# Kernel tuning notes

Hardware: AMD Instinct MI355X
Metric: run time of the kernel (lower is better)

Reference implementation:

```python
import jax, jax.numpy as jnp
import numpy as np

NUM_HEADS = 16
HEAD_DIM = 64  # att_output_dim // num_heads = 1024 // 16


def setup_inputs() -> dict:
    key = jax.random.key(0)
    ks = jax.random.split(key, 7)
    B, S, D_IN, D_OUT = 4, 2048, 1024, 1024
    std = 1.0 / np.sqrt(D_IN)
    return {
        "ts10_input": jax.random.normal(ks[0], (B, S, D_IN), dtype=jnp.float32),
        "Wq": jax.random.uniform(ks[1], (D_IN, D_OUT), jnp.float32, -std, std),
        "bq": jax.random.uniform(ks[2], (D_OUT,), jnp.float32, -std, std),
        "Wk": jax.random.uniform(ks[3], (D_IN, D_OUT), jnp.float32, -std, std),
        "bk": jax.random.uniform(ks[4], (D_OUT,), jnp.float32, -std, std),
        "Wv": jax.random.uniform(ks[5], (D_IN, D_OUT), jnp.float32, -std, std),
        "bv": jax.random.uniform(ks[6], (D_OUT,), jnp.float32, -std, std),
        "mask": 1,
    }


def reference(ts10_input, Wq, bq, Wk, bk, Wv, bv, mask):
    B, S, _ = ts10_input.shape
    H, Dh = NUM_HEADS, HEAD_DIM

    def split_heads(x):  # (B,S,H*Dh) -> (B,H,S,Dh)
        return x.reshape(B, S, H, Dh).transpose(0, 2, 1, 3)

    q = split_heads(ts10_input @ Wq + bq)
    k = split_heads(ts10_input @ Wk + bk)
    v = split_heads(ts10_input @ Wv + bv)

    scores = jnp.einsum("bhqd,bhkd->bhqk", q, k) / jnp.sqrt(jnp.float32(Dh))
    if mask:
        causal = jnp.tril(jnp.ones((S, S), dtype=bool))  # keep lower triangle incl diag
        scores = jnp.where(causal, scores, -jnp.inf)
    probs = jax.nn.softmax(scores, axis=-1)
    ctx = jnp.einsum("bhqk,bhkd->bhqd", probs, v)
    return ctx.transpose(0, 2, 1, 3).reshape(B, S, H * Dh)
```

## Files before the change

### kernel.cpp

```cpp
#include <hip/hip_runtime.h>

typedef __bf16 bf16x8 __attribute__((ext_vector_type(8)));
typedef __bf16 bf16x4 __attribute__((ext_vector_type(4)));
typedef short s16x4 __attribute__((ext_vector_type(4)));
typedef float f32x4 __attribute__((ext_vector_type(4)));
typedef unsigned short u16x8 __attribute__((ext_vector_type(8)));
typedef unsigned short u16x4 __attribute__((ext_vector_type(4)));
typedef unsigned int u32x2 __attribute__((ext_vector_type(2)));
typedef unsigned int u32x4 __attribute__((ext_vector_type(4)));
typedef unsigned int __attribute__((address_space(1))) as1_uint;
typedef unsigned int __attribute__((address_space(3))) as3_uint;

#define S_LEN 2048
#define NB 4
#define NH 16
#define HD 64
#define DM 1024

#define Q_SCALE 0.18033688011112042f

__device__ __forceinline__ unsigned short f2bf(float f) {
  union { float f; unsigned int u; } v; v.f = f;
  unsigned int r = v.u + 0x7fffu + ((v.u >> 16) & 1u);
  return (unsigned short)(r >> 16);
}

__device__ __forceinline__ unsigned int fbits(float f) {
  union { float f; unsigned int u; } v; v.f = f;
  return v.u;
}

__device__ __forceinline__ f32x4 mfma16(u16x4 a, u16x4 b, f32x4 c) {
#if __has_builtin(__builtin_amdgcn_mfma_f32_16x16x16_bf16)
  return __builtin_amdgcn_mfma_f32_16x16x16_bf16(
      __builtin_bit_cast(bf16x4, a), __builtin_bit_cast(bf16x4, b), c, 0, 0, 0);
#else
  return __builtin_amdgcn_mfma_f32_16x16x16bf16_1k(
      __builtin_bit_cast(s16x4, a), __builtin_bit_cast(s16x4, b), c, 0, 0, 0);
#endif
}

__global__ __launch_bounds__(256) void cvt_x(const float* __restrict__ x,
                                             unsigned short* __restrict__ xb) {
  int i = (blockIdx.x * 256 + threadIdx.x) * 8;
  f32x4 a = *(const f32x4*)(x + i);
  f32x4 b = *(const f32x4*)(x + i + 4);
  u16x8 o;
  o[0] = f2bf(a[0]); o[1] = f2bf(a[1]); o[2] = f2bf(a[2]); o[3] = f2bf(a[3]);
  o[4] = f2bf(b[0]); o[5] = f2bf(b[1]); o[6] = f2bf(b[2]); o[7] = f2bf(b[3]);
  *(u16x8*)(xb + i) = o;
}

__global__ __launch_bounds__(256) void cvt_wt(const float* __restrict__ Wq,
                                              const float* __restrict__ Wk,
                                              const float* __restrict__ Wv,
                                              unsigned short* __restrict__ wt) {
  const float* W = (blockIdx.z == 0) ? Wq : (blockIdx.z == 1) ? Wk : Wv;
  unsigned short* WT = wt + (size_t)blockIdx.z * DM * DM;
  __shared__ float tile[32][33];
  int tx = threadIdx.x & 31, ty = threadIdx.x >> 5;
  int k0 = blockIdx.x * 32, n0 = blockIdx.y * 32;
#pragma unroll
  for (int i = 0; i < 4; ++i)
    tile[ty + 8 * i][tx] = W[(size_t)(k0 + ty + 8 * i) * DM + n0 + tx];
  __syncthreads();
#pragma unroll
  for (int i = 0; i < 4; ++i)
    WT[(size_t)(n0 + ty + 8 * i) * DM + k0 + tx] = f2bf(tile[tx][ty + 8 * i]);
}

__global__ __launch_bounds__(256, 4) void qkv_gemm(const unsigned short* __restrict__ xb,
                                                   const unsigned short* __restrict__ wt,
                                                   const float* __restrict__ bq,
                                                   const float* __restrict__ bk,
                                                   const float* __restrict__ bv,
                                                   unsigned short* __restrict__ qo,
                                                   unsigned short* __restrict__ ko,
                                                   unsigned short* __restrict__ vto) {
  const int z = blockIdx.z;
  const unsigned short* WT = wt + (size_t)z * DM * DM;
  const float* bias = (z == 0) ? bq : (z == 1) ? bk : bv;
  const int m0 = blockIdx.x * 128;
  const int n0 = blockIdx.y * 128;
  __shared__ __align__(16) unsigned short Lds[128 * 136];
  unsigned short* Al = Lds;
  unsigned short* Bl = Lds + 128 * 64;
  const int tid = threadIdx.x;
  const int wave = tid >> 6, lane = tid & 63, quad = lane >> 4, lw = lane & 15;
  const int wm = (wave >> 1) * 64, wn = (wave & 1) * 64;

  f32x4 acc[4][4];
#pragma unroll
  for (int mt = 0; mt < 4; ++mt)
#pragma unroll
    for (int nt = 0; nt < 4; ++nt) acc[mt][nt] = (f32x4){0.f, 0.f, 0.f, 0.f};

  for (int k0 = 0; k0 < DM; k0 += 64) {
    __syncthreads();
#pragma unroll
    for (int i = 0; i < 4; ++i) {
      int idx = i * 256 + tid;
      int r = idx >> 3, cp = idx & 7;
      int cl = cp ^ (r & 7);
      const unsigned short* ga = xb + (size_t)(m0 + r) * DM + k0 + cl * 8;
      __builtin_amdgcn_global_load_lds((const as1_uint*)ga, (as3_uint*)(Al + idx * 8), 16, 0, 0);
      const unsigned short* gb = WT + (size_t)(n0 + r) * DM + k0 + cl * 8;
      __builtin_amdgcn_global_load_lds((const as1_uint*)gb, (as3_uint*)(Bl + idx * 8), 16, 0, 0);
    }
    __syncthreads();
#pragma unroll
    for (int kc = 0; kc < 2; ++kc) {
      bf16x8 af[4], bfr[4];
#pragma unroll
      for (int mt = 0; mt < 4; ++mt) {
        int r = wm + mt * 16 + lw;
        int cp = (kc * 4 + quad) ^ (r & 7);
        af[mt] = *(const bf16x8*)(Al + r * 64 + cp * 8);
      }
#pragma unroll
      for (int nt = 0; nt < 4; ++nt) {
        int r = wn + nt * 16 + lw;
        int cp = (kc * 4 + quad) ^ (r & 7);
        bfr[nt] = *(const bf16x8*)(Bl + r * 64 + cp * 8);
      }
#pragma unroll
      for (int mt = 0; mt < 4; ++mt)
#pragma unroll
        for (int nt = 0; nt < 4; ++nt)
          acc[mt][nt] = __builtin_amdgcn_mfma_f32_16x16x32_bf16(af[mt], bfr[nt], acc[mt][nt], 0, 0, 0);
    }
  }

  float bias4[4];
#pragma unroll
  for (int nt = 0; nt < 4; ++nt) bias4[nt] = bias[n0 + wn + nt * 16 + lw];

  __syncthreads();

  if (z < 2) {
    const float sc = (z == 0) ? Q_SCALE : 1.0f;
#pragma unroll
    for (int mt = 0; mt < 4; ++mt)
#pragma unroll
      for (int nt = 0; nt < 4; ++nt) {
        int n = wn + nt * 16 + lw;
#pragma unroll
        for (int r = 0; r < 4; ++r) {
          int m = wm + mt * 16 + quad * 4 + r;
          Lds[m * 136 + n] = f2bf((acc[mt][nt][r] + bias4[nt]) * sc);
        }
      }
    __syncthreads();
    unsigned short* dst = (z == 0) ? qo : ko;
    const int rr = tid >> 1;
    const int cbase = (tid & 1) * 64;
    const int m = m0 + rr;
    const int b = m >> 11, s = m & 2047;
#pragma unroll
    for (int ch = 0; ch < 8; ++ch) {
      int cc = cbase + ch * 8;
      int n = n0 + cc;
      int h = n >> 6, d = n & 63;
      u32x4 v = *(const u32x4*)(Lds + rr * 136 + cc);
      *(u32x4*)(dst + ((size_t)(b * NH + h) * S_LEN + s) * HD + d) = v;
    }
  } else {
#pragma unroll
    for (int mt = 0; mt < 4; ++mt)
#pragma unroll
      for (int nt = 0; nt < 4; ++nt) {
        int n = wn + nt * 16 + lw;
        int mb = wm + mt * 16 + quad * 4;
        u16x4 pk;
#pragma unroll
        for (int r = 0; r < 4; ++r) pk[r] = f2bf(acc[mt][nt][r] + bias4[nt]);
        *(u16x4*)(Lds + n * 136 + mb) = pk;
      }
    __syncthreads();
    const int rr = tid >> 1;
    const int cbase = (tid & 1) * 64;
    const int n = n0 + rr;
    const int h = n >> 6, d = n & 63;
#pragma unroll
    for (int ch = 0; ch < 8; ++ch) {
      int cc = cbase + ch * 8;
      int m = m0 + cc;
      int b = m >> 11, s = m & 2047;
      u32x4 v = *(const u32x4*)(Lds + rr * 136 + cc);
      *(u32x4*)(vto + ((size_t)(b * NH + h) * HD + d) * S_LEN + s) = v;
    }
  }
}

__global__ __launch_bounds__(256, 4) void attn(const unsigned short* __restrict__ Qb,
                                               const unsigned short* __restrict__ Kb,
                                               const unsigned short* __restrict__ Vtb,
                                               float* __restrict__ out) {
  const int flat = blockIdx.x;
  const int bh_lo = flat & 7;
  const int qpair = (flat >> 3) & 15;
  const int bh_hi = flat >> 7;
  const int bh = bh_lo + 8 * bh_hi;
  const int b = bh >> 4, h = bh & 15;
  const int tid = threadIdx.x;
  const int wave = tid >> 6, lane = tid & 63;
  const int quad = lane >> 4, lw = lane & 15;
  const int qlo = qpair * 64;
  const int qhi = (31 - qpair) * 64;
  const unsigned short* Qp = Qb + (size_t)bh * S_LEN * HD;
  const unsigned short* Kp = Kb + (size_t)bh * S_LEN * HD;
  const unsigned short* Vp = Vtb + (size_t)bh * HD * S_LEN;

  __shared__ __align__(16) unsigned short Kl[2][64 * 64];
  __shared__ __align__(16) unsigned short Vl[2][64 * 64];

  bf16x8 aq[2][2];
#pragma unroll
  for (int rg = 0; rg < 2; ++rg) {
    const int qbase = rg ? qhi : qlo;
#pragma unroll
    for (int kc = 0; kc < 2; ++kc)
      aq[rg][kc] = *(const bf16x8*)(Qp + (size_t)(qbase + wave * 16 + lw) * HD + kc * 32 + quad * 8);
  }

  u16x4 ones4;
#pragma unroll
  for (int i = 0; i < 4; ++i) ones4[i] = 0x3F80;

  f32x4 accO[2][4];
  f32x4 accL[2];
#pragma unroll
  for (int rg = 0; rg < 2; ++rg) {
    accL[rg] = (f32x4){0.f, 0.f, 0.f, 0.f};
#pragma unroll
    for (int dg = 0; dg < 4; ++dg) accO[rg][dg] = (f32x4){0.f, 0.f, 0.f, 0.f};
  }

  const int qr0 = qlo + wave * 16 + lw;
  const int qr1 = qhi + wave * 16 + lw;

  const int T = 32 - qpair;

  {
#pragma unroll
    for (int i = 0; i < 2; ++i) {
      int idx = i * 256 + tid;
      int r = idx >> 3, c = (idx & 7) ^ (r & 7);
      __builtin_amdgcn_global_load_lds((const as1_uint*)(Kp + (size_t)r * HD + c * 8),
                                       (as3_uint*)(Kl[0] + idx * 8), 16, 0, 0);
      __builtin_amdgcn_global_load_lds((const as1_uint*)(Vp + (size_t)r * S_LEN + c * 8),
                                       (as3_uint*)(Vl[0] + idx * 8), 16, 0, 0);
    }
  }

  for (int t = 0; t < T; ++t) {
    const int kv = t * 64;
    const int cur = t & 1;
    __syncthreads();

    if (t + 1 < T) {
      const int kvn = kv + 64;
#pragma unroll
      for (int i = 0; i < 2; ++i) {
        int idx = i * 256 + tid;
        int r = idx >> 3, c = (idx & 7) ^ (r & 7);
        __builtin_amdgcn_global_load_lds((const as1_uint*)(Kp + (size_t)(kvn + r) * HD + c * 8),
                                         (as3_uint*)(Kl[cur ^ 1] + idx * 8), 16, 0, 0);
        __builtin_amdgcn_global_load_lds((const as1_uint*)(Vp + (size_t)r * S_LEN + kvn + c * 8),
                                         (as3_uint*)(Vl[cur ^ 1] + idx * 8), 16, 0, 0);
      }
    }

    const bool a0 = (t <= qpair);
    const bool d0 = (t == qpair);
    const bool d1 = (t == T - 1);

#pragma unroll
    for (int g = 0; g < 4; ++g) {
      const unsigned short* kp = Kl[cur] + (g * 16 + lw) * 64;
      const int sw = lw & 7;
      bf16x8 kf0 = *(const bf16x8*)(kp + ((quad ^ sw) * 8));
      bf16x8 kf1 = *(const bf16x8*)(kp + (((4 + quad) ^ sw) * 8));

      u16x4 pf[2];
#pragma unroll
      for (int rg = 0; rg < 2; ++rg) {
        if (rg == 0 && !a0) continue;
        f32x4 s = (f32x4){0.f, 0.f, 0.f, 0.f};
        s = __builtin_amdgcn_mfma_f32_16x16x32_bf16(kf0, aq[rg][0], s, 0, 0, 0);
        s = __builtin_amdgcn_mfma_f32_16x16x32_bf16(kf1, aq[rg][1], s, 0, 0, 0);
        const bool dg_ = rg ? d1 : d0;
        const int qr = rg ? qr1 : qr0;
        if (dg_) {
#pragma unroll
          for (int r = 0; r < 4; ++r) {
            float e = __builtin_amdgcn_exp2f(s[r]);
            s[r] = (kv + g * 16 + quad * 4 + r > qr) ? 0.f : e;
          }
        } else {
#pragma unroll
          for (int r = 0; r < 4; ++r) s[r] = __builtin_amdgcn_exp2f(s[r]);
        }
        u32x2 pk;
        pk[0] = (fbits(s[1]) & 0xFFFF0000u) | (fbits(s[0]) >> 16);
        pk[1] = (fbits(s[3]) & 0xFFFF0000u) | (fbits(s[2]) >> 16);
        pf[rg] = __builtin_bit_cast(u16x4, pk);
      }

#pragma unroll
      for (int dg = 0; dg < 4; ++dg) {
        const int row = dg * 16 + lw;
        const int slot = (2 * g + (quad >> 1)) ^ (lw & 7);
        u16x4 vf = *(const u16x4*)(Vl[cur] + row * 64 + slot * 8 + (quad & 1) * 4);
        if (a0) accO[0][dg] = mfma16(pf[0], vf, accO[0][dg]);
        accO[1][dg] = mfma16(pf[1], vf, accO[1][dg]);
      }
      if (a0) accL[0] = mfma16(pf[0], ones4, accL[0]);
      accL[1] = mfma16(pf[1], ones4, accL[1]);
    }
  }

#pragma unroll
  for (int rg = 0; rg < 2; ++rg) {
    const int qbase = rg ? qhi : qlo;
    float* op = out + ((size_t)b * S_LEN + qbase + wave * 16 + quad * 4) * DM + h * HD + lw;
#pragma unroll
    for (int r = 0; r < 4; ++r) {
      float inv = 1.0f / accL[rg][r];
#pragma unroll
      for (int dg = 0; dg < 4; ++dg) op[(size_t)r * DM + dg * 16] = accO[rg][dg][r] * inv;
    }
  }
}

extern "C" void kernel_launch(void* const* d_in, const int* in_sizes, int n_in,
                              void* d_out, int out_size, void* d_ws, size_t ws_size,
                              hipStream_t stream) {
  const float* x = (const float*)d_in[0];
  const float* Wq = (const float*)d_in[1];
  const float* bq = (const float*)d_in[2];
  const float* Wk = (const float*)d_in[3];
  const float* bk = (const float*)d_in[4];
  const float* Wv = (const float*)d_in[5];
  const float* bv = (const float*)d_in[6];
  float* out = (float*)d_out;

  char* ws = (char*)d_ws;
  unsigned short* xb = (unsigned short*)(ws + 0);
  unsigned short* wt = (unsigned short*)(ws + 16777216);
  unsigned short* qb = (unsigned short*)(ws + 23068672);
  unsigned short* kb = (unsigned short*)(ws + 39845888);
  unsigned short* vt = (unsigned short*)(ws + 56623104);

  hipLaunchKernelGGL(cvt_x, dim3(4096), dim3(256), 0, stream, x, xb);
  hipLaunchKernelGGL(cvt_wt, dim3(32, 32, 3), dim3(256), 0, stream, Wq, Wk, Wv, wt);
  hipLaunchKernelGGL(qkv_gemm, dim3(64, 8, 3), dim3(256), 0, stream,
                     xb, wt, bq, bk, bv, qb, kb, vt);
  hipLaunchKernelGGL(attn, dim3(1024), dim3(256), 0, stream, qb, kb, vt, out);
}
```

Measured before the change: 230.1 us.

## Double-buffer QKV GEMM LDS staging and merge conversion kernels into one launch

The QKV GEMM K-loop now uses two 32-wide LDS buffers, issuing the next tile's global-to-LDS loads before computing on the current one. This drops one barrier per iteration and overlaps memory with MFMA work. It also changes the swizzle pattern to fit the narrower tile. Separately, the x conversion and weight transpose-conversion kernels are fused into one launch, which removes one kernel launch at the cost of a branch per block. The LDS layout reuse and the smaller K step double the loop iterations, so per-iteration overhead goes up.

After: 226.0 us. About the same (-1.8%).

```diff
diff --git a/kernel.cpp b/kernel.cpp
--- a/kernel.cpp
+++ b/kernel.cpp
@@ -40,33 +40,36 @@
 #endif
 }
 
-__global__ __launch_bounds__(256) void cvt_x(const float* __restrict__ x,
-                                             unsigned short* __restrict__ xb) {
-  int i = (blockIdx.x * 256 + threadIdx.x) * 8;
-  f32x4 a = *(const f32x4*)(x + i);
-  f32x4 b = *(const f32x4*)(x + i + 4);
-  u16x8 o;
-  o[0] = f2bf(a[0]); o[1] = f2bf(a[1]); o[2] = f2bf(a[2]); o[3] = f2bf(a[3]);
-  o[4] = f2bf(b[0]); o[5] = f2bf(b[1]); o[6] = f2bf(b[2]); o[7] = f2bf(b[3]);
-  *(u16x8*)(xb + i) = o;
-}
-
-__global__ __launch_bounds__(256) void cvt_wt(const float* __restrict__ Wq,
-                                              const float* __restrict__ Wk,
-                                              const float* __restrict__ Wv,
-                                              unsigned short* __restrict__ wt) {
-  const float* W = (blockIdx.z == 0) ? Wq : (blockIdx.z == 1) ? Wk : Wv;
-  unsigned short* WT = wt + (size_t)blockIdx.z * DM * DM;
+__global__ __launch_bounds__(256) void prep(const float* __restrict__ x,
+                                            unsigned short* __restrict__ xb,
+                                            const float* __restrict__ Wq,
+                                            const float* __restrict__ Wk,
+                                            const float* __restrict__ Wv,
+                                            unsigned short* __restrict__ wt) {
   __shared__ float tile[32][33];
-  int tx = threadIdx.x & 31, ty = threadIdx.x >> 5;
-  int k0 = blockIdx.x * 32, n0 = blockIdx.y * 32;
-#pragma unroll
-  for (int i = 0; i < 4; ++i)
-    tile[ty + 8 * i][tx] = W[(size_t)(k0 + ty + 8 * i) * DM + n0 + tx];
-  __syncthreads();
-#pragma unroll
-  for (int i = 0; i < 4; ++i)
-    WT[(size_t)(n0 + ty + 8 * i) * DM + k0 + tx] = f2bf(tile[tx][ty + 8 * i]);
+  if (blockIdx.x < 4096) {
+    int i = (blockIdx.x * 256 + threadIdx.x) * 8;
+    f32x4 a = *(const f32x4*)(x + i);
+    f32x4 b = *(const f32x4*)(x + i + 4);
+    u16x8 o;
+    o[0] = f2bf(a[0]); o[1] = f2bf(a[1]); o[2] = f2bf(a[2]); o[3] = f2bf(a[3]);
+    o[4] = f2bf(b[0]); o[5] = f2bf(b[1]); o[6] = f2bf(b[2]); o[7] = f2bf(b[3]);
+    *(u16x8*)(xb + i) = o;
+  } else {
+    int id = blockIdx.x - 4096;
+    int z = id >> 10, r = id & 1023;
+    const float* W = (z == 0) ? Wq : (z == 1) ? Wk : Wv;
+    unsigned short* WT = wt + (size_t)z * DM * DM;
+    int k0 = (r & 31) * 32, n0 = (r >> 5) * 32;
+    int tx = threadIdx.x & 31, ty = threadIdx.x >> 5;
+#pragma unroll
+    for (int i = 0; i < 4; ++i)
+      tile[ty + 8 * i][tx] = W[(size_t)(k0 + ty + 8 * i) * DM + n0 + tx];
+    __syncthreads();
+#pragma unroll
+    for (int i = 0; i < 4; ++i)
+      WT[(size_t)(n0 + ty + 8 * i) * DM + k0 + tx] = f2bf(tile[tx][ty + 8 * i]);
+  }
 }
 
 __global__ __launch_bounds__(256, 4) void qkv_gemm(const unsigned short* __restrict__ xb,
@@ -83,8 +86,6 @@
   const int m0 = blockIdx.x * 128;
   const int n0 = blockIdx.y * 128;
   __shared__ __align__(16) unsigned short Lds[128 * 136];
-  unsigned short* Al = Lds;
-  unsigned short* Bl = Lds + 128 * 64;
   const int tid = threadIdx.x;
   const int wave = tid >> 6, lane = tid & 63, quad = lane >> 4, lw = lane & 15;
   const int wm = (wave >> 1) * 64, wn = (wave & 1) * 64;
@@ -95,40 +96,45 @@
 #pragma unroll
     for (int nt = 0; nt < 4; ++nt) acc[mt][nt] = (f32x4){0.f, 0.f, 0.f, 0.f};
 
-  for (int k0 = 0; k0 < DM; k0 += 64) {
-    __syncthreads();
-#pragma unroll
-    for (int i = 0; i < 4; ++i) {
-      int idx = i * 256 + tid;
-      int r = idx >> 3, cp = idx & 7;
-      int cl = cp ^ (r & 7);
-      const unsigned short* ga = xb + (size_t)(m0 + r) * DM + k0 + cl * 8;
-      __builtin_amdgcn_global_load_lds((const as1_uint*)ga, (as3_uint*)(Al + idx * 8), 16, 0, 0);
-      const unsigned short* gb = WT + (size_t)(n0 + r) * DM + k0 + cl * 8;
-      __builtin_amdgcn_global_load_lds((const as1_uint*)gb, (as3_uint*)(Bl + idx * 8), 16, 0, 0);
-    }
-    __syncthreads();
-#pragma unroll
-    for (int kc = 0; kc < 2; ++kc) {
-      bf16x8 af[4], bfr[4];
-#pragma unroll
-      for (int mt = 0; mt < 4; ++mt) {
-        int r = wm + mt * 16 + lw;
-        int cp = (kc * 4 + quad) ^ (r & 7);
-        af[mt] = *(const bf16x8*)(Al + r * 64 + cp * 8);
-      }
-#pragma unroll
-      for (int nt = 0; nt < 4; ++nt) {
-        int r = wn + nt * 16 + lw;
-        int cp = (kc * 4 + quad) ^ (r & 7);
-        bfr[nt] = *(const bf16x8*)(Bl + r * 64 + cp * 8);
-      }
-#pragma unroll
-      for (int mt = 0; mt < 4; ++mt)
-#pragma unroll
-        for (int nt = 0; nt < 4; ++nt)
-          acc[mt][nt] = __builtin_amdgcn_mfma_f32_16x16x32_bf16(af[mt], bfr[nt], acc[mt][nt], 0, 0, 0);
-    }
+  auto stage = [&](int k0, int buf) {
+    unsigned short* Al = Lds + buf * 4096;
+    unsigned short* Bl = Lds + 8192 + buf * 4096;
+#pragma unroll
+    for (int i = 0; i < 2; ++i) {
+      int c = i * 256 + tid;
+      int row = c >> 2;
+      int scn = (c & 3) ^ ((row >> 1) & 3);
+      const unsigned short* ga = xb + (size_t)(m0 + row) * DM + k0 + scn * 8;
+      __builtin_amdgcn_global_load_lds((const as1_uint*)ga, (as3_uint*)(Al + c * 8), 16, 0, 0);
+      const unsigned short* gb = WT + (size_t)(n0 + row) * DM + k0 + scn * 8;
+      __builtin_amdgcn_global_load_lds((const as1_uint*)gb, (as3_uint*)(Bl + c * 8), 16, 0, 0);
+    }
+  };
+
+  stage(0, 0);
+  for (int k0 = 0; k0 < DM; k0 += 32) {
+    const int cur = (k0 >> 5) & 1;
+    __syncthreads();
+    if (k0 + 32 < DM) stage(k0 + 32, cur ^ 1);
+
+    const unsigned short* Al = Lds + cur * 4096;
+    const unsigned short* Bl = Lds + 8192 + cur * 4096;
+    bf16x8 af[4], bfr[4];
+#pragma unroll
+    for (int mt = 0; mt < 4; ++mt) {
+      int r = wm + mt * 16 + lw;
+      af[mt] = *(const bf16x8*)(Al + r * 32 + (quad ^ ((r >> 1) & 3)) * 8);
+    }
+#pragma unroll
+    for (int nt = 0; nt < 4; ++nt) {
+      int r = wn + nt * 16 + lw;
+      bfr[nt] = *(const bf16x8*)(Bl + r * 32 + (quad ^ ((r >> 1) & 3)) * 8);
+    }
+#pragma unroll
+    for (int mt = 0; mt < 4; ++mt)
+#pragma unroll
+      for (int nt = 0; nt < 4; ++nt)
+        acc[mt][nt] = __builtin_amdgcn_mfma_f32_16x16x32_bf16(af[mt], bfr[nt], acc[mt][nt], 0, 0, 0);
   }
 
   float bias4[4];
@@ -352,8 +358,7 @@
   unsigned short* kb = (unsigned short*)(ws + 39845888);
   unsigned short* vt = (unsigned short*)(ws + 56623104);
 
-  hipLaunchKernelGGL(cvt_x, dim3(4096), dim3(256), 0, stream, x, xb);
-  hipLaunchKernelGGL(cvt_wt, dim3(32, 32, 3), dim3(256), 0, stream, Wq, Wk, Wv, wt);
+  hipLaunchKernelGGL(prep, dim3(7168), dim3(256), 0, stream, x, xb, Wq, Wk, Wv, wt);
   hipLaunchKernelGGL(qkv_gemm, dim3(64, 8, 3), dim3(256), 0, stream,
                      xb, wt, bq, bk, bv, qb, kb, vt);
   hipLaunchKernelGGL(attn, dim3(1024), dim3(256), 0, stream, qb, kb, vt, out);
```

## Merge conversion kernels and halve GEMM epilogue LDS to raise occupancy

Applied to the files above, without the earlier changes.

Combines the x-to-bf16 conversion and the weight transpose-convert into one launch, which removes a kernel launch and the gap between the two kernels. In the QKV GEMM, the epilogue staging now runs in two phases of 64 rows or columns, so LDS shrinks from 128x136 to 16384 halves and launch bounds rise to 5 blocks per SIMD group. The goal is higher GEMM occupancy. The cost is an extra pair of barriers in the epilogue, with half the waves idle during each staging phase.

New measurement: 267.7 us. 16.4% more time.

```diff
diff --git a/kernel.cpp b/kernel.cpp
--- a/kernel.cpp
+++ b/kernel.cpp
@@ -40,36 +40,39 @@
 #endif
 }
 
-__global__ __launch_bounds__(256) void cvt_x(const float* __restrict__ x,
-                                             unsigned short* __restrict__ xb) {
-  int i = (blockIdx.x * 256 + threadIdx.x) * 8;
-  f32x4 a = *(const f32x4*)(x + i);
-  f32x4 b = *(const f32x4*)(x + i + 4);
-  u16x8 o;
-  o[0] = f2bf(a[0]); o[1] = f2bf(a[1]); o[2] = f2bf(a[2]); o[3] = f2bf(a[3]);
-  o[4] = f2bf(b[0]); o[5] = f2bf(b[1]); o[6] = f2bf(b[2]); o[7] = f2bf(b[3]);
-  *(u16x8*)(xb + i) = o;
-}
-
-__global__ __launch_bounds__(256) void cvt_wt(const float* __restrict__ Wq,
-                                              const float* __restrict__ Wk,
-                                              const float* __restrict__ Wv,
-                                              unsigned short* __restrict__ wt) {
-  const float* W = (blockIdx.z == 0) ? Wq : (blockIdx.z == 1) ? Wk : Wv;
-  unsigned short* WT = wt + (size_t)blockIdx.z * DM * DM;
+__global__ __launch_bounds__(256) void prep(const float* __restrict__ x,
+                                            unsigned short* __restrict__ xb,
+                                            const float* __restrict__ Wq,
+                                            const float* __restrict__ Wk,
+                                            const float* __restrict__ Wv,
+                                            unsigned short* __restrict__ wt) {
   __shared__ float tile[32][33];
-  int tx = threadIdx.x & 31, ty = threadIdx.x >> 5;
-  int k0 = blockIdx.x * 32, n0 = blockIdx.y * 32;
-#pragma unroll
-  for (int i = 0; i < 4; ++i)
-    tile[ty + 8 * i][tx] = W[(size_t)(k0 + ty + 8 * i) * DM + n0 + tx];
-  __syncthreads();
-#pragma unroll
-  for (int i = 0; i < 4; ++i)
-    WT[(size_t)(n0 + ty + 8 * i) * DM + k0 + tx] = f2bf(tile[tx][ty + 8 * i]);
-}
-
-__global__ __launch_bounds__(256, 4) void qkv_gemm(const unsigned short* __restrict__ xb,
+  if (blockIdx.x < 4096) {
+    int i = (blockIdx.x * 256 + threadIdx.x) * 8;
+    f32x4 a = *(const f32x4*)(x + i);
+    f32x4 b = *(const f32x4*)(x + i + 4);
+    u16x8 o;
+    o[0] = f2bf(a[0]); o[1] = f2bf(a[1]); o[2] = f2bf(a[2]); o[3] = f2bf(a[3]);
+    o[4] = f2bf(b[0]); o[5] = f2bf(b[1]); o[6] = f2bf(b[2]); o[7] = f2bf(b[3]);
+    *(u16x8*)(xb + i) = o;
+  } else {
+    int id = blockIdx.x - 4096;
+    int z = id >> 10, r = id & 1023;
+    const float* W = (z == 0) ? Wq : (z == 1) ? Wk : Wv;
+    unsigned short* WT = wt + (size_t)z * DM * DM;
+    int k0 = (r & 31) * 32, n0 = (r >> 5) * 32;
+    int tx = threadIdx.x & 31, ty = threadIdx.x >> 5;
+#pragma unroll
+    for (int i = 0; i < 4; ++i)
+      tile[ty + 8 * i][tx] = W[(size_t)(k0 + ty + 8 * i) * DM + n0 + tx];
+    __syncthreads();
+#pragma unroll
+    for (int i = 0; i < 4; ++i)
+      WT[(size_t)(n0 + ty + 8 * i) * DM + k0 + tx] = f2bf(tile[tx][ty + 8 * i]);
+  }
+}
+
+__global__ __launch_bounds__(256, 5) void qkv_gemm(const unsigned short* __restrict__ xb,
                                                    const unsigned short* __restrict__ wt,
                                                    const float* __restrict__ bq,
                                                    const float* __restrict__ bk,
@@ -82,9 +85,9 @@
   const float* bias = (z == 0) ? bq : (z == 1) ? bk : bv;
   const int m0 = blockIdx.x * 128;
   const int n0 = blockIdx.y * 128;
-  __shared__ __align__(16) unsigned short Lds[128 * 136];
+  __shared__ __align__(16) unsigned short Lds[16384];
   unsigned short* Al = Lds;
-  unsigned short* Bl = Lds + 128 * 64;
+  unsigned short* Bl = Lds + 8192;
   const int tid = threadIdx.x;
   const int wave = tid >> 6, lane = tid & 63, quad = lane >> 4, lw = lane & 15;
   const int wm = (wave >> 1) * 64, wn = (wave & 1) * 64;
@@ -135,59 +138,69 @@
 #pragma unroll
   for (int nt = 0; nt < 4; ++nt) bias4[nt] = bias[n0 + wn + nt * 16 + lw];
 
-  __syncthreads();
-
   if (z < 2) {
     const float sc = (z == 0) ? Q_SCALE : 1.0f;
-#pragma unroll
-    for (int mt = 0; mt < 4; ++mt)
-#pragma unroll
-      for (int nt = 0; nt < 4; ++nt) {
-        int n = wn + nt * 16 + lw;
-#pragma unroll
-        for (int r = 0; r < 4; ++r) {
-          int m = wm + mt * 16 + quad * 4 + r;
-          Lds[m * 136 + n] = f2bf((acc[mt][nt][r] + bias4[nt]) * sc);
-        }
-      }
-    __syncthreads();
     unsigned short* dst = (z == 0) ? qo : ko;
-    const int rr = tid >> 1;
-    const int cbase = (tid & 1) * 64;
-    const int m = m0 + rr;
-    const int b = m >> 11, s = m & 2047;
-#pragma unroll
-    for (int ch = 0; ch < 8; ++ch) {
-      int cc = cbase + ch * 8;
-      int n = n0 + cc;
-      int h = n >> 6, d = n & 63;
-      u32x4 v = *(const u32x4*)(Lds + rr * 136 + cc);
-      *(u32x4*)(dst + ((size_t)(b * NH + h) * S_LEN + s) * HD + d) = v;
+#pragma unroll
+    for (int ph = 0; ph < 2; ++ph) {
+      __syncthreads();
+      if ((wave >> 1) == ph) {
+#pragma unroll
+        for (int mt = 0; mt < 4; ++mt)
+#pragma unroll
+          for (int nt = 0; nt < 4; ++nt) {
+            int n = wn + nt * 16 + lw;
+#pragma unroll
+            for (int r = 0; r < 4; ++r) {
+              int mloc = mt * 16 + quad * 4 + r;
+              Lds[mloc * 136 + n] = f2bf((acc[mt][nt][r] + bias4[nt]) * sc);
+            }
+          }
+      }
+      __syncthreads();
+      const int rr = tid >> 2;
+      const int cbase = (tid & 3) * 32;
+      const int m = m0 + ph * 64 + rr;
+      const int b = m >> 11, s = m & 2047;
+#pragma unroll
+      for (int ch = 0; ch < 4; ++ch) {
+        int cc = cbase + ch * 8;
+        int n = n0 + cc;
+        int h = n >> 6, d = n & 63;
+        u32x4 v = *(const u32x4*)(Lds + rr * 136 + cc);
+        *(u32x4*)(dst + ((size_t)(b * NH + h) * S_LEN + s) * HD + d) = v;
+      }
     }
   } else {
 #pragma unroll
-    for (int mt = 0; mt < 4; ++mt)
-#pragma unroll
-      for (int nt = 0; nt < 4; ++nt) {
-        int n = wn + nt * 16 + lw;
-        int mb = wm + mt * 16 + quad * 4;
-        u16x4 pk;
-#pragma unroll
-        for (int r = 0; r < 4; ++r) pk[r] = f2bf(acc[mt][nt][r] + bias4[nt]);
-        *(u16x4*)(Lds + n * 136 + mb) = pk;
-      }
-    __syncthreads();
-    const int rr = tid >> 1;
-    const int cbase = (tid & 1) * 64;
-    const int n = n0 + rr;
-    const int h = n >> 6, d = n & 63;
-#pragma unroll
-    for (int ch = 0; ch < 8; ++ch) {
-      int cc = cbase + ch * 8;
-      int m = m0 + cc;
-      int b = m >> 11, s = m & 2047;
-      u32x4 v = *(const u32x4*)(Lds + rr * 136 + cc);
-      *(u32x4*)(vto + ((size_t)(b * NH + h) * HD + d) * S_LEN + s) = v;
+    for (int ph = 0; ph < 2; ++ph) {
+      __syncthreads();
+      if ((wave & 1) == ph) {
+#pragma unroll
+        for (int mt = 0; mt < 4; ++mt)
+#pragma unroll
+          for (int nt = 0; nt < 4; ++nt) {
+            int nloc = nt * 16 + lw;
+            int mb = wm + mt * 16 + quad * 4;
+            u16x4 pk;
+#pragma unroll
+            for (int r = 0; r < 4; ++r) pk[r] = f2bf(acc[mt][nt][r] + bias4[nt]);
+            *(u16x4*)(Lds + nloc * 136 + mb) = pk;
+          }
+      }
+      __syncthreads();
+      const int rr = tid >> 2;
+      const int cbase = (tid & 3) * 32;
+      const int n = n0 + ph * 64 + rr;
+      const int h = n >> 6, d = n & 63;
+#pragma unroll
+      for (int ch = 0; ch < 4; ++ch) {
+        int cc = cbase + ch * 8;
+        int m = m0 + cc;
+        int b = m >> 11, s = m & 2047;
+        u32x4 v = *(const u32x4*)(Lds + rr * 136 + cc);
+        *(u32x4*)(vto + ((size_t)(b * NH + h) * HD + d) * S_LEN + s) = v;
+      }
     }
   }
 }
@@ -352,8 +365,7 @@
   unsigned short* kb = (unsigned short*)(ws + 39845888);
   unsigned short* vt = (unsigned short*)(ws + 56623104);
 
-  hipLaunchKernelGGL(cvt_x, dim3(4096), dim3(256), 0, stream, x, xb);
-  hipLaunchKernelGGL(cvt_wt, dim3(32, 32, 3), dim3(256), 0, stream, Wq, Wk, Wv, wt);
+  hipLaunchKernelGGL(prep, dim3(7168), dim3(256), 0, stream, x, xb, Wq, Wk, Wv, wt);
   hipLaunchKernelGGL(qkv_gemm, dim3(64, 8, 3), dim3(256), 0, stream,
                      xb, wt, bq, bk, bv, qb, kb, vt);
   hipLaunchKernelGGL(attn, dim3(1024), dim3(256), 0, stream, qb, kb, vt, out);
```
